# Optimization experiments

Hardware: AMD Instinct MI355X
Metric: run time of the kernel (lower is better)

The kernel has to match this reference:

```python
import jax, jax.numpy as jnp
import numpy as np

EPS = 1e-5
SCALE = 30.0

def _ln(x, g, b):
    m = jnp.mean(x, axis=-1, keepdims=True)
    v = jnp.mean((x - m) ** 2, axis=-1, keepdims=True)
    return (x - m) * jax.lax.rsqrt(v + EPS) * g + b

def setup_inputs() -> dict:
    key = jax.random.key(0)
    ks = jax.random.split(key, 12)
    B, L, K, H, NIN = 4, 2048, 48, 128, 512
    s = 0.02
    return {
        "h_V": jax.random.normal(ks[0], (B, L, H), jnp.float32),
        "h_E": jax.random.normal(ks[1], (B, L, K, NIN - H), jnp.float32),
        "mask_V": jnp.ones((B, L), jnp.float32),
        "mask_E": jnp.ones((B, L, K), jnp.float32),
        "w1": jax.random.normal(ks[2], (NIN, H), jnp.float32) * s,
        "b1": jnp.zeros((H,), jnp.float32),
        "w2": jax.random.normal(ks[3], (H, H), jnp.float32) * s,
        "b2": jnp.zeros((H,), jnp.float32),
        "w3": jax.random.normal(ks[4], (H, H), jnp.float32) * s,
        "b3": jnp.zeros((H,), jnp.float32),
        "g1": jnp.ones((H,), jnp.float32),
        "bn1": jnp.zeros((H,), jnp.float32),
        "g2": jnp.ones((H,), jnp.float32),
        "bn2": jnp.zeros((H,), jnp.float32),
        "wf1": jax.random.normal(ks[5], (H, 4 * H), jnp.float32) * s,
        "bf1": jnp.zeros((4 * H,), jnp.float32),
        "wf2": jax.random.normal(ks[6], (4 * H, H), jnp.float32) * s,
        "bf2": jnp.zeros((H,), jnp.float32),
    }

def reference(h_V, h_E, mask_V, mask_E, w1, b1, w2, b2, w3, b3, g1, bn1, g2, bn2, wf1, bf1, wf2, bf2):
    B, L, H = h_V.shape
    K = h_E.shape[-2]
    gelu = lambda x: jax.nn.gelu(x, approximate=False)  # torch nn.GELU default (erf)
    # expand source node over K neighbors and concat: (B,L,K,num_in)
    h_V_exp = jnp.broadcast_to(h_V[:, :, None, :], (B, L, K, H))
    h_EV = jnp.concatenate([h_V_exp, h_E], axis=-1)
    h_msg = gelu(jnp.einsum('blki,ih->blkh', h_EV, w1) + b1)
    h_msg = gelu(jnp.einsum('blkh,hj->blkj', h_msg, w2) + b2)
    h_msg = jnp.einsum('blkh,hj->blkj', h_msg, w3) + b3
    h_msg = mask_E[..., None] * h_msg
    dh = jnp.sum(h_msg, axis=-2) / SCALE  # masked sum-aggregate over K
    h = _ln(h_V + dh, g1, bn1)
    dff = jnp.einsum('blh,hf->blf', h, wf1) + bf1
    dff = jnp.einsum('blf,fh->blh', gelu(dff), wf2) + bf2
    h = _ln(h + dff, g2, bn2)
    return mask_V[..., None] * h
```

## Files before the change

kernel.cpp:

```cpp
#include <hip/hip_runtime.h>
#include <hip/hip_bf16.h>


typedef __bf16 bf16x8 __attribute__((ext_vector_type(8)));
typedef __bf16 bf16x4 __attribute__((ext_vector_type(4)));
typedef float f32x4 __attribute__((ext_vector_type(4)));

#define HH 128
#define EE 384
#define KK 48

__device__ __forceinline__ float gelu_f(float x) {
  float x2 = x * x;
  float u = x * (-1.5957691216f - 0.0713548163f * x2);
  float e = __expf(u);
  return __fdividef(x, 1.0f + e);
}

__device__ __forceinline__ bf16x8 cvt8v(f32x4 a, f32x4 b) {
  bf16x8 r;
  #pragma unroll
  for (int i = 0; i < 4; ++i) { r[i] = (__bf16)a[i]; r[i + 4] = (__bf16)b[i]; }
  return r;
}

__device__ __forceinline__ f32x4 mfma16(bf16x8 a, bf16x8 b, f32x4 c) {
  return __builtin_amdgcn_mfma_f32_16x16x32_bf16(a, b, c, 0, 0, 0);
}

__device__ __forceinline__ void gload16(const void* g, void* l) {
  __builtin_amdgcn_global_load_lds(
      (const __attribute__((address_space(1))) void*)g,
      (__attribute__((address_space(3))) void*)l, 16, 0, 0);
}

__global__ void prep_kernel(const float* __restrict__ w1, const float* __restrict__ w2,
                            const float* __restrict__ w3, const float* __restrict__ wf1,
                            const float* __restrict__ wf2, __bf16* __restrict__ out) {
  int idx = blockIdx.x * 256 + threadIdx.x;
  if (idx < 49152) {
    int t = idx & 7, lane = (idx >> 3) & 63, n = (idx >> 9) & 7, kc = idx >> 12;
    int e = kc * 32 + (lane >> 4) * 8 + t, h = n * 16 + (lane & 15);
    out[idx] = (__bf16)w1[(128 + e) * 128 + h];
  } else if (idx < 65536) {
    int u = idx - 49152;
    int t = u & 7, lane = (u >> 3) & 63, n = (u >> 9) & 7, kc = u >> 12;
    int e = kc * 32 + (lane >> 4) * 8 + t, h = n * 16 + (lane & 15);
    out[idx] = (__bf16)w2[e * 128 + h];
  } else if (idx < 81920) {
    int u = idx - 65536;
    int t = u & 7, lane = (u >> 3) & 63, n = (u >> 9) & 7, kc = u >> 12;
    int e = kc * 32 + (lane >> 4) * 8 + t, h = n * 16 + (lane & 15);
    out[idx] = (__bf16)w3[e * 128 + h];
  } else if (idx < 147456) {
    int u = idx - 81920;
    int t = u & 7, lane = (u >> 3) & 63, n = (u >> 9) & 7, kc = (u >> 12) & 3, w = u >> 14;
    int f = w * 128 + n * 16 + (lane & 15), h = kc * 32 + (lane >> 4) * 8 + t;
    out[idx] = (__bf16)wf1[h * 512 + f];
  } else if (idx < 212992) {
    int u = idx - 147456;
    int t = u & 7, lane = (u >> 3) & 63, n = (u >> 9) & 1, kc = (u >> 10) & 15, w = u >> 14;
    int j = w * 32 + n * 16 + (lane & 15), f = kc * 32 + (lane >> 4) * 8 + t;
    out[idx] = (__bf16)wf2[f * 128 + j];
  }
}

__global__ __launch_bounds__(128) void v1_kernel(const float* __restrict__ hV,
                                                 const float* __restrict__ w1,
                                                 const float* __restrict__ b1,
                                                 float* __restrict__ V1) {
  __shared__ __align__(16) float sV[16][128];
  const int tid = threadIdx.x;
  const long p0 = (long)blockIdx.x * 16;
  for (int i = 0; i < 16; ++i) sV[i][tid] = hV[(p0 + i) * HH + tid];
  __syncthreads();
  float acc[16];
  float bb = b1[tid];
  #pragma unroll
  for (int p = 0; p < 16; ++p) acc[p] = bb;
  for (int k = 0; k < 128; k += 4) {
    float wa = w1[(k + 0) * HH + tid];
    float wb = w1[(k + 1) * HH + tid];
    float wc = w1[(k + 2) * HH + tid];
    float wd = w1[(k + 3) * HH + tid];
    #pragma unroll
    for (int p = 0; p < 16; ++p) {
      float4 h4 = *(const float4*)&sV[p][k];
      acc[p] = fmaf(h4.x, wa, fmaf(h4.y, wb, fmaf(h4.z, wc, fmaf(h4.w, wd, acc[p]))));
    }
  }
  #pragma unroll
  for (int p = 0; p < 16; ++p) V1[(p0 + p) * HH + tid] = acc[p];
}

__global__ __launch_bounds__(256, 4) void msg_kernel(
    const float* __restrict__ hE, const float* __restrict__ hV,
    const float* __restrict__ maskE,
    const __bf16* __restrict__ w1f, const __bf16* __restrict__ w2f,
    const __bf16* __restrict__ w3f, const float* __restrict__ V1,
    const float* __restrict__ b2, const float* __restrict__ b3,
    const float* __restrict__ g1, const float* __restrict__ bn1,
    float* __restrict__ outH) {
  __shared__ __align__(16) char sBuf[3][12288];
  __shared__ __align__(16) float sBias[512];
  __shared__ __align__(16) float sPart[4][2];

  const int tid = threadIdx.x;
  const int lane = tid & 63;
  const int w = tid >> 6;
  const int fr = lane & 15;
  const int fg = lane >> 4;
  const long p = blockIdx.x;

  for (int j = tid; j < 512; j += 256) {
    float v;
    if (j < 128) v = b2[j];
    else if (j < 256) v = b3[j - 128];
    else if (j < 384) v = g1[j - 256];
    else v = bn1[j - 384];
    sBias[j] = v;
  }
  __syncthreads();

  const float mk0 = maskE[p * KK + fr];
  const float mk1 = maskE[p * KK + 16 + fr];
  const float mk2 = maskE[p * KK + 32 + fr];

  const char* hEp = (const char*)(hE + p * (long)(KK * EE));
  const int lrow = lane >> 4;
  const int lcb = (lane & 15) * 16;
  const int r0 = (w * 3 + 0) * 4 + lrow;
  const int r1 = (w * 3 + 1) * 4 + lrow;
  const int r2 = (w * 3 + 2) * 4 + lrow;
  const char* srcA0 = hEp + r0 * 1536 + (lcb ^ ((r0 & 7) << 5));
  const char* srcA1 = hEp + r1 * 1536 + (lcb ^ ((r1 & 7) << 5));
  const char* srcA2 = hEp + r2 * 1536 + (lcb ^ ((r2 & 7) << 5));
  const int dst0 = (w * 3 + 0) * 1024;
  const int dst1 = (w * 3 + 1) * 1024;
  const int dst2 = (w * 3 + 2) * 1024;

  const __bf16* b1base = w1f + (2 * w) * 512 + lane * 8;
  const __bf16* b2base = w2f + (2 * w) * 512 + lane * 8;
  const __bf16* b3base = w3f + (2 * w) * 512 + lane * 8;

  const int aswz = (fr & 7) << 5;
  const int hswz = (fr & 7) << 4;
  char* hB = &sBuf[0][0];

  f32x4 acc[3][2];
  #pragma unroll
  for (int m = 0; m < 3; ++m)
    #pragma unroll
    for (int n = 0; n < 2; ++n) acc[m][n] = (f32x4){0.f, 0.f, 0.f, 0.f};

  bf16x8 Bs0[2], Bs1[2], Bs2[2], Bs3[2];

#define STAGE(C, BUF) { \
    gload16(srcA0 + (C) * 256, &sBuf[BUF][0] + dst0); \
    gload16(srcA1 + (C) * 256, &sBuf[BUF][0] + dst1); \
    gload16(srcA2 + (C) * 256, &sBuf[BUF][0] + dst2); }
#define LOADB(SET, BASE, KC) { \
    SET[0] = *(const bf16x8*)((BASE) + (KC) * 4096); \
    SET[1] = *(const bf16x8*)((BASE) + (KC) * 4096 + 256); }
#define WAITV(N) asm volatile("s_waitcnt vmcnt(" #N ")" ::: "memory")
#define BAR      asm volatile("s_barrier" ::: "memory")
#define BARL     asm volatile("s_waitcnt lgkmcnt(0)\ns_barrier" ::: "memory")

#define KSTEP(BUF, KS, SET) { \
    const char* rb_ = &sBuf[BUF][0]; \
    const int cb_ = ((KS) * 128 + fg * 32) ^ aswz; \
    f32x4 x0_ = *(const f32x4*)(rb_ + fr * 256 + cb_); \
    f32x4 x1_ = *(const f32x4*)(rb_ + fr * 256 + cb_ + 16); \
    f32x4 x2_ = *(const f32x4*)(rb_ + (16 + fr) * 256 + cb_); \
    f32x4 x3_ = *(const f32x4*)(rb_ + (16 + fr) * 256 + cb_ + 16); \
    f32x4 x4_ = *(const f32x4*)(rb_ + (32 + fr) * 256 + cb_); \
    f32x4 x5_ = *(const f32x4*)(rb_ + (32 + fr) * 256 + cb_ + 16); \
    bf16x8 af0 = cvt8v(x0_, x1_); \
    bf16x8 af1 = cvt8v(x2_, x3_); \
    bf16x8 af2 = cvt8v(x4_, x5_); \
    acc[0][0] = mfma16(SET[0], af0, acc[0][0]); acc[0][1] = mfma16(SET[1], af0, acc[0][1]); \
    acc[1][0] = mfma16(SET[0], af1, acc[1][0]); acc[1][1] = mfma16(SET[1], af1, acc[1][1]); \
    acc[2][0] = mfma16(SET[0], af2, acc[2][0]); acc[2][1] = mfma16(SET[1], af2, acc[2][1]); }

#define KSTEPH(KS, SET) { \
    const int cb_ = ((KS) * 64 + fg * 16) ^ hswz; \
    bf16x8 af0 = *(const bf16x8*)(hB + fr * 256 + cb_); \
    bf16x8 af1 = *(const bf16x8*)(hB + (16 + fr) * 256 + cb_); \
    bf16x8 af2 = *(const bf16x8*)(hB + (32 + fr) * 256 + cb_); \
    acc[0][0] = mfma16(SET[0], af0, acc[0][0]); acc[0][1] = mfma16(SET[1], af0, acc[0][1]); \
    acc[1][0] = mfma16(SET[0], af1, acc[1][0]); acc[1][1] = mfma16(SET[1], af1, acc[1][1]); \
    acc[2][0] = mfma16(SET[0], af2, acc[2][0]); acc[2][1] = mfma16(SET[1], af2, acc[2][1]); }

#define EPI(BQ0, BQ1) { \
    _Pragma("unroll") for (int m_ = 0; m_ < 3; ++m_) { \
      const int rb_ = (m_ * 16 + fr) * 256; \
      { bf16x4 t_; \
        _Pragma("unroll") for (int j_ = 0; j_ < 4; ++j_) t_[j_] = (__bf16)gelu_f(acc[m_][0][j_] + BQ0[j_]); \
        *(bf16x4*)(hB + rb_ + (((2 * w) * 32 + fg * 8) ^ hswz)) = t_; \
        acc[m_][0] = (f32x4){0.f, 0.f, 0.f, 0.f}; } \
      { bf16x4 t_; \
        _Pragma("unroll") for (int j_ = 0; j_ < 4; ++j_) t_[j_] = (__bf16)gelu_f(acc[m_][1][j_] + BQ1[j_]); \
        *(bf16x4*)(hB + rb_ + (((2 * w + 1) * 32 + fg * 8) ^ hswz)) = t_; \
        acc[m_][1] = (f32x4){0.f, 0.f, 0.f, 0.f}; } } }

  STAGE(0, 0);
  LOADB(Bs0, b1base, 0);
  LOADB(Bs1, b1base, 1);
  STAGE(1, 1);
  LOADB(Bs2, b1base, 2);
  LOADB(Bs3, b1base, 3);

  f32x4 vq0, vq1, hq0, hq1;

  WAITV(7); BAR;
  KSTEP(0, 0, Bs0); LOADB(Bs0, b1base, 4);
  KSTEP(0, 1, Bs1); LOADB(Bs1, b1base, 5);
  STAGE(2, 2);

  WAITV(7); BAR;
  KSTEP(1, 0, Bs2); LOADB(Bs2, b1base, 6);
  KSTEP(1, 1, Bs3); LOADB(Bs3, b1base, 7);
  STAGE(3, 0);

  WAITV(7); BAR;
  KSTEP(2, 0, Bs0); LOADB(Bs0, b1base, 8);
  KSTEP(2, 1, Bs1); LOADB(Bs1, b1base, 9);
  STAGE(4, 1);

  WAITV(7); BAR;
  KSTEP(0, 0, Bs2); LOADB(Bs2, b1base, 10);
  KSTEP(0, 1, Bs3); LOADB(Bs3, b1base, 11);
  STAGE(5, 2);

  WAITV(7); BAR;
  KSTEP(1, 0, Bs0); LOADB(Bs0, b2base, 0);
  vq0 = *(const f32x4*)(V1 + p * HH + (2 * w) * 16 + fg * 4);
  vq1 = *(const f32x4*)(V1 + p * HH + (2 * w + 1) * 16 + fg * 4);
  KSTEP(1, 1, Bs1); LOADB(Bs1, b2base, 1);

  WAITV(6); BAR;
  KSTEP(2, 0, Bs2); LOADB(Bs2, b2base, 2);
  KSTEP(2, 1, Bs3); LOADB(Bs3, b2base, 3);

  WAITV(4);
  EPI(vq0, vq1);
  BARL;

  KSTEPH(0, Bs0); LOADB(Bs0, b3base, 0);
  KSTEPH(1, Bs1); LOADB(Bs1, b3base, 1);
  WAITV(4);
  KSTEPH(2, Bs2); LOADB(Bs2, b3base, 2);
  KSTEPH(3, Bs3); LOADB(Bs3, b3base, 3);
  BARL;
  {
    f32x4 bq0 = *(const f32x4*)(&sBias[(2 * w) * 16 + fg * 4]);
    f32x4 bq1 = *(const f32x4*)(&sBias[(2 * w + 1) * 16 + fg * 4]);
    EPI(bq0, bq1);
  }
  BARL;

  WAITV(6);
  KSTEPH(0, Bs0);
  hq0 = *(const f32x4*)(hV + p * HH + (2 * w) * 16 + fg * 4);
  hq1 = *(const f32x4*)(hV + p * HH + (2 * w + 1) * 16 + fg * 4);
  KSTEPH(1, Bs1);
  WAITV(4);
  KSTEPH(2, Bs2);
  KSTEPH(3, Bs3);

  f32x4 red[2];
  {
    #pragma unroll
    for (int n = 0; n < 2; ++n) {
      f32x4 bq = *(const f32x4*)(&sBias[128 + (2 * w + n) * 16 + fg * 4]);
      red[n] = mk0 * (acc[0][n] + bq) + mk1 * (acc[1][n] + bq) + mk2 * (acc[2][n] + bq);
    }
    #pragma unroll
    for (int off = 1; off <= 8; off <<= 1)
      #pragma unroll
      for (int n = 0; n < 2; ++n)
        #pragma unroll
        for (int j = 0; j < 4; ++j)
          red[n][j] += __shfl_xor(red[n][j], off);
  }

  WAITV(0);
  {
    f32x4 xq[2];
    xq[0] = hq0 + red[0] * (1.f / 30.f);
    xq[1] = hq1 + red[1] * (1.f / 30.f);
    float s = 0.f, t = 0.f;
    #pragma unroll
    for (int n = 0; n < 2; ++n)
      #pragma unroll
      for (int j = 0; j < 4; ++j) { float x = xq[n][j]; s += x; t += x * x; }
    s += __shfl_xor(s, 16); s += __shfl_xor(s, 32);
    t += __shfl_xor(t, 16); t += __shfl_xor(t, 32);
    if (lane == 0) { sPart[w][0] = s; sPart[w][1] = t; }
    BARL;
    float S = sPart[0][0] + sPart[1][0] + sPart[2][0] + sPart[3][0];
    float T = sPart[0][1] + sPart[1][1] + sPart[2][1] + sPart[3][1];
    float mean = S * (1.f / 128.f);
    float var = T * (1.f / 128.f) - mean * mean;
    float rs = rsqrtf(var + 1e-5f);
    if (fr == 0) {
      #pragma unroll
      for (int n = 0; n < 2; ++n) {
        f32x4 gq = *(const f32x4*)(&sBias[256 + (2 * w + n) * 16 + fg * 4]);
        f32x4 bq = *(const f32x4*)(&sBias[384 + (2 * w + n) * 16 + fg * 4]);
        f32x4 o;
        #pragma unroll
        for (int j = 0; j < 4; ++j) o[j] = (xq[n][j] - mean) * rs * gq[j] + bq[j];
        *(f32x4*)(outH + p * HH + (2 * w + n) * 16 + fg * 4) = o;
      }
    }
  }
#undef STAGE
#undef LOADB
#undef WAITV
#undef BAR
#undef BARL
#undef KSTEP
#undef KSTEPH
#undef EPI
}

__global__ __launch_bounds__(256, 2) void ffn_kernel(
    const float* __restrict__ xin, const __bf16* __restrict__ wf1g,
    const float* __restrict__ bf1, const __bf16* __restrict__ wf2g,
    const float* __restrict__ bf2, const float* __restrict__ g2,
    const float* __restrict__ bn2, const float* __restrict__ maskV,
    float* __restrict__ out) {
  __shared__ __align__(16) __bf16 sX[16][136];
  __shared__ __align__(16) __bf16 sH1[16][520];
  __shared__ __align__(16) float sOut[16][132];
  const int tid = threadIdx.x, lane = tid & 63, w = tid >> 6;
  const long row0 = (long)blockIdx.x * 16;
  const int fr = lane & 15, fg = lane >> 4;
  const __bf16* bw1 = wf1g + w * 16384 + lane * 8;
  const __bf16* bw2 = wf2g + w * 16384 + lane * 8;

  {
    int r = tid >> 4, c = (tid & 15) * 8;
    const float* src = xin + (row0 + r) * HH + c;
    f32x4 v0 = *(const f32x4*)src, v1 = *(const f32x4*)(src + 4);
    *(bf16x8*)&sX[r][c] = cvt8v(v0, v1);
  }
  __syncthreads();

  f32x4 a1[8];
  #pragma unroll
  for (int n = 0; n < 8; ++n) a1[n] = (f32x4){0.f, 0.f, 0.f, 0.f};
  #pragma unroll
  for (int kc = 0; kc < 4; ++kc) {
    int k0 = kc * 32;
    bf16x8 af0 = *(const bf16x8*)&sX[fr][k0 + fg * 8];
    #pragma unroll
    for (int n = 0; n < 8; ++n) {
      bf16x8 bfr = *(const bf16x8*)(bw1 + (kc * 8 + n) * 512);
      a1[n] = mfma16(af0, bfr, a1[n]);
    }
  }
  #pragma unroll
  for (int n = 0; n < 8; ++n) {
    float bv = bf1[w * 128 + n * 16 + fr];
    #pragma unroll
    for (int j = 0; j < 4; ++j)
      sH1[fg * 4 + j][w * 128 + n * 16 + fr] = (__bf16)gelu_f(a1[n][j] + bv);
  }
  __syncthreads();

  f32x4 a2[2];
  #pragma unroll
  for (int n = 0; n < 2; ++n) a2[n] = (f32x4){0.f, 0.f, 0.f, 0.f};
  #pragma unroll
  for (int kc = 0; kc < 16; ++kc) {
    int k0 = kc * 32;
    bf16x8 af0 = *(const bf16x8*)&sH1[fr][k0 + fg * 8];
    #pragma unroll
    for (int n = 0; n < 2; ++n) {
      bf16x8 bfr = *(const bf16x8*)(bw2 + (kc * 2 + n) * 512);
      a2[n] = mfma16(af0, bfr, a2[n]);
    }
  }
  #pragma unroll
  for (int n = 0; n < 2; ++n) {
    float bv = bf2[w * 32 + n * 16 + fr];
    #pragma unroll
    for (int j = 0; j < 4; ++j)
      sOut[fg * 4 + j][w * 32 + n * 16 + fr] = a2[n][j] + bv;
  }
  __syncthreads();

  {
    int r = tid >> 4, c0 = (tid & 15) * 8;
    long p = row0 + r;
    const float* xp = xin + p * HH + c0;
    float x[8];
    #pragma unroll
    for (int i = 0; i < 8; ++i) x[i] = xp[i] + sOut[r][c0 + i];
    float s = 0.f;
    #pragma unroll
    for (int i = 0; i < 8; ++i) s += x[i];
    s += __shfl_xor(s, 1); s += __shfl_xor(s, 2); s += __shfl_xor(s, 4); s += __shfl_xor(s, 8);
    float mean = s * (1.f / 128.f);
    float q = 0.f;
    #pragma unroll
    for (int i = 0; i < 8; ++i) { float e = x[i] - mean; q += e * e; }
    q += __shfl_xor(q, 1); q += __shfl_xor(q, 2); q += __shfl_xor(q, 4); q += __shfl_xor(q, 8);
    float rs = rsqrtf(q * (1.f / 128.f) + 1e-5f);
    float mv = maskV[p];
    float* op = out + p * HH + c0;
    #pragma unroll
    for (int i = 0; i < 8; ++i)
      op[i] = ((x[i] - mean) * rs * g2[c0 + i] + bn2[c0 + i]) * mv;
  }
}

extern "C" void kernel_launch(void* const* d_in, const int* in_sizes, int n_in,
                              void* d_out, int out_size, void* d_ws, size_t ws_size,
                              hipStream_t stream) {
  const float* hV    = (const float*)d_in[0];
  const float* hE    = (const float*)d_in[1];
  const float* maskV = (const float*)d_in[2];
  const float* maskE = (const float*)d_in[3];
  const float* w1    = (const float*)d_in[4];
  const float* b1    = (const float*)d_in[5];
  const float* w2    = (const float*)d_in[6];
  const float* b2    = (const float*)d_in[7];
  const float* w3    = (const float*)d_in[8];
  const float* b3    = (const float*)d_in[9];
  const float* g1    = (const float*)d_in[10];
  const float* bn1   = (const float*)d_in[11];
  const float* g2    = (const float*)d_in[12];
  const float* bn2   = (const float*)d_in[13];
  const float* wf1   = (const float*)d_in[14];
  const float* bf1   = (const float*)d_in[15];
  const float* wf2   = (const float*)d_in[16];
  const float* bf2   = (const float*)d_in[17];
  float* out = (float*)d_out;

  __bf16* wsb = (__bf16*)d_ws;
  float* V1   = (float*)((char*)d_ws + 425984);
  float* hbuf = (float*)((char*)d_ws + 4620288);

  prep_kernel<<<832, 256, 0, stream>>>(w1, w2, w3, wf1, wf2, wsb);
  v1_kernel<<<512, 128, 0, stream>>>(hV, w1, b1, V1);
  msg_kernel<<<8192, 256, 0, stream>>>(hE, hV, maskE,
                                       wsb, wsb + 49152, wsb + 65536, V1,
                                       b2, b3, g1, bn1, hbuf);
  ffn_kernel<<<512, 256, 0, stream>>>(hbuf, wsb + 81920, bf1, wsb + 147456, bf2,
                                      g2, bn2, maskV, out);
}
```

Before: 200.2 us.

## Split message kernel into layer-1 and layers-2/3 kernels via bf16 workspace

Splits the fused message MLP kernel into two kernels. The first streams h_E, computes layer 1 plus GELU and writes the bf16 hidden activations to a workspace buffer. The second processes four positions per block, keeping the W2 and W3 fragments in registers and double-buffering the hidden tiles. The point is to stop reloading W2/W3 for every position and to let each phase run at its own occupancy. The cost is an extra global round-trip of about 100MB of bf16 intermediates. The split path is used only when the workspace is large enough, otherwise the original fused kernel runs.

```diff
diff --git a/kernel.cpp b/kernel.cpp
--- a/kernel.cpp
+++ b/kernel.cpp
@@ -93,69 +93,7 @@
   for (int p = 0; p < 16; ++p) V1[(p0 + p) * HH + tid] = acc[p];
 }
 
-__global__ __launch_bounds__(256, 4) void msg_kernel(
-    const float* __restrict__ hE, const float* __restrict__ hV,
-    const float* __restrict__ maskE,
-    const __bf16* __restrict__ w1f, const __bf16* __restrict__ w2f,
-    const __bf16* __restrict__ w3f, const float* __restrict__ V1,
-    const float* __restrict__ b2, const float* __restrict__ b3,
-    const float* __restrict__ g1, const float* __restrict__ bn1,
-    float* __restrict__ outH) {
-  __shared__ __align__(16) char sBuf[3][12288];
-  __shared__ __align__(16) float sBias[512];
-  __shared__ __align__(16) float sPart[4][2];
-
-  const int tid = threadIdx.x;
-  const int lane = tid & 63;
-  const int w = tid >> 6;
-  const int fr = lane & 15;
-  const int fg = lane >> 4;
-  const long p = blockIdx.x;
-
-  for (int j = tid; j < 512; j += 256) {
-    float v;
-    if (j < 128) v = b2[j];
-    else if (j < 256) v = b3[j - 128];
-    else if (j < 384) v = g1[j - 256];
-    else v = bn1[j - 384];
-    sBias[j] = v;
-  }
-  __syncthreads();
-
-  const float mk0 = maskE[p * KK + fr];
-  const float mk1 = maskE[p * KK + 16 + fr];
-  const float mk2 = maskE[p * KK + 32 + fr];
-
-  const char* hEp = (const char*)(hE + p * (long)(KK * EE));
-  const int lrow = lane >> 4;
-  const int lcb = (lane & 15) * 16;
-  const int r0 = (w * 3 + 0) * 4 + lrow;
-  const int r1 = (w * 3 + 1) * 4 + lrow;
-  const int r2 = (w * 3 + 2) * 4 + lrow;
-  const char* srcA0 = hEp + r0 * 1536 + (lcb ^ ((r0 & 7) << 5));
-  const char* srcA1 = hEp + r1 * 1536 + (lcb ^ ((r1 & 7) << 5));
-  const char* srcA2 = hEp + r2 * 1536 + (lcb ^ ((r2 & 7) << 5));
-  const int dst0 = (w * 3 + 0) * 1024;
-  const int dst1 = (w * 3 + 1) * 1024;
-  const int dst2 = (w * 3 + 2) * 1024;
-
-  const __bf16* b1base = w1f + (2 * w) * 512 + lane * 8;
-  const __bf16* b2base = w2f + (2 * w) * 512 + lane * 8;
-  const __bf16* b3base = w3f + (2 * w) * 512 + lane * 8;
-
-  const int aswz = (fr & 7) << 5;
-  const int hswz = (fr & 7) << 4;
-  char* hB = &sBuf[0][0];
-
-  f32x4 acc[3][2];
-  #pragma unroll
-  for (int m = 0; m < 3; ++m)
-    #pragma unroll
-    for (int n = 0; n < 2; ++n) acc[m][n] = (f32x4){0.f, 0.f, 0.f, 0.f};
-
-  bf16x8 Bs0[2], Bs1[2], Bs2[2], Bs3[2];
-
-#define STAGE(C, BUF) { \
+#define STAGEM(C, BUF) { \
     gload16(srcA0 + (C) * 256, &sBuf[BUF][0] + dst0); \
     gload16(srcA1 + (C) * 256, &sBuf[BUF][0] + dst1); \
     gload16(srcA2 + (C) * 256, &sBuf[BUF][0] + dst2); }
@@ -165,8 +103,7 @@
 #define WAITV(N) asm volatile("s_waitcnt vmcnt(" #N ")" ::: "memory")
 #define BAR      asm volatile("s_barrier" ::: "memory")
 #define BARL     asm volatile("s_waitcnt lgkmcnt(0)\ns_barrier" ::: "memory")
-
-#define KSTEP(BUF, KS, SET) { \
+#define KSTEPM(BUF, KS, SET) { \
     const char* rb_ = &sBuf[BUF][0]; \
     const int cb_ = ((KS) * 128 + fg * 32) ^ aswz; \
     f32x4 x0_ = *(const f32x4*)(rb_ + fr * 256 + cb_); \
@@ -181,92 +118,341 @@
     acc[0][0] = mfma16(SET[0], af0, acc[0][0]); acc[0][1] = mfma16(SET[1], af0, acc[0][1]); \
     acc[1][0] = mfma16(SET[0], af1, acc[1][0]); acc[1][1] = mfma16(SET[1], af1, acc[1][1]); \
     acc[2][0] = mfma16(SET[0], af2, acc[2][0]); acc[2][1] = mfma16(SET[1], af2, acc[2][1]); }
-
-#define KSTEPH(KS, SET) { \
+#define KSTEPH2(HB, KS, SET) { \
     const int cb_ = ((KS) * 64 + fg * 16) ^ hswz; \
-    bf16x8 af0 = *(const bf16x8*)(hB + fr * 256 + cb_); \
-    bf16x8 af1 = *(const bf16x8*)(hB + (16 + fr) * 256 + cb_); \
-    bf16x8 af2 = *(const bf16x8*)(hB + (32 + fr) * 256 + cb_); \
+    bf16x8 af0 = *(const bf16x8*)((HB) + fr * 256 + cb_); \
+    bf16x8 af1 = *(const bf16x8*)((HB) + (16 + fr) * 256 + cb_); \
+    bf16x8 af2 = *(const bf16x8*)((HB) + (32 + fr) * 256 + cb_); \
     acc[0][0] = mfma16(SET[0], af0, acc[0][0]); acc[0][1] = mfma16(SET[1], af0, acc[0][1]); \
     acc[1][0] = mfma16(SET[0], af1, acc[1][0]); acc[1][1] = mfma16(SET[1], af1, acc[1][1]); \
     acc[2][0] = mfma16(SET[0], af2, acc[2][0]); acc[2][1] = mfma16(SET[1], af2, acc[2][1]); }
-
-#define EPI(BQ0, BQ1) { \
+#define EPI2(HB, BQ0, BQ1) { \
     _Pragma("unroll") for (int m_ = 0; m_ < 3; ++m_) { \
       const int rb_ = (m_ * 16 + fr) * 256; \
       { bf16x4 t_; \
         _Pragma("unroll") for (int j_ = 0; j_ < 4; ++j_) t_[j_] = (__bf16)gelu_f(acc[m_][0][j_] + BQ0[j_]); \
-        *(bf16x4*)(hB + rb_ + (((2 * w) * 32 + fg * 8) ^ hswz)) = t_; \
+        *(bf16x4*)((HB) + rb_ + (((2 * w) * 32 + fg * 8) ^ hswz)) = t_; \
         acc[m_][0] = (f32x4){0.f, 0.f, 0.f, 0.f}; } \
       { bf16x4 t_; \
         _Pragma("unroll") for (int j_ = 0; j_ < 4; ++j_) t_[j_] = (__bf16)gelu_f(acc[m_][1][j_] + BQ1[j_]); \
-        *(bf16x4*)(hB + rb_ + (((2 * w + 1) * 32 + fg * 8) ^ hswz)) = t_; \
+        *(bf16x4*)((HB) + rb_ + (((2 * w + 1) * 32 + fg * 8) ^ hswz)) = t_; \
         acc[m_][1] = (f32x4){0.f, 0.f, 0.f, 0.f}; } } }
 
-  STAGE(0, 0);
+__global__ __launch_bounds__(256, 4) void msg1_kernel(
+    const float* __restrict__ hE, const __bf16* __restrict__ w1f,
+    const float* __restrict__ V1, char* __restrict__ h1g) {
+  __shared__ __align__(16) char sBuf[3][12288];
+  const int tid = threadIdx.x;
+  const int lane = tid & 63;
+  const int w = tid >> 6;
+  const int fr = lane & 15;
+  const int fg = lane >> 4;
+  const long p = blockIdx.x;
+
+  const char* hEp = (const char*)(hE + p * (long)(KK * EE));
+  const int lrow = lane >> 4;
+  const int lcb = (lane & 15) * 16;
+  const int r0 = (w * 3 + 0) * 4 + lrow;
+  const int r1 = (w * 3 + 1) * 4 + lrow;
+  const int r2 = (w * 3 + 2) * 4 + lrow;
+  const char* srcA0 = hEp + r0 * 1536 + (lcb ^ ((r0 & 7) << 5));
+  const char* srcA1 = hEp + r1 * 1536 + (lcb ^ ((r1 & 7) << 5));
+  const char* srcA2 = hEp + r2 * 1536 + (lcb ^ ((r2 & 7) << 5));
+  const int dst0 = (w * 3 + 0) * 1024;
+  const int dst1 = (w * 3 + 1) * 1024;
+  const int dst2 = (w * 3 + 2) * 1024;
+  const __bf16* b1base = w1f + (2 * w) * 512 + lane * 8;
+  const int aswz = (fr & 7) << 5;
+  const int hswz = (fr & 7) << 4;
+  char* hB = &sBuf[0][0];
+
+  f32x4 acc[3][2];
+  #pragma unroll
+  for (int m = 0; m < 3; ++m)
+    #pragma unroll
+    for (int n = 0; n < 2; ++n) acc[m][n] = (f32x4){0.f, 0.f, 0.f, 0.f};
+  bf16x8 Bs0[2], Bs1[2], Bs2[2], Bs3[2];
+
+  STAGEM(0, 0);
   LOADB(Bs0, b1base, 0);
   LOADB(Bs1, b1base, 1);
-  STAGE(1, 1);
+  STAGEM(1, 1);
   LOADB(Bs2, b1base, 2);
   LOADB(Bs3, b1base, 3);
 
-  f32x4 vq0, vq1, hq0, hq1;
-
-  WAITV(7); BAR;
-  KSTEP(0, 0, Bs0); LOADB(Bs0, b1base, 4);
-  KSTEP(0, 1, Bs1); LOADB(Bs1, b1base, 5);
-  STAGE(2, 2);
-
-  WAITV(7); BAR;
-  KSTEP(1, 0, Bs2); LOADB(Bs2, b1base, 6);
-  KSTEP(1, 1, Bs3); LOADB(Bs3, b1base, 7);
-  STAGE(3, 0);
-
-  WAITV(7); BAR;
-  KSTEP(2, 0, Bs0); LOADB(Bs0, b1base, 8);
-  KSTEP(2, 1, Bs1); LOADB(Bs1, b1base, 9);
-  STAGE(4, 1);
-
-  WAITV(7); BAR;
-  KSTEP(0, 0, Bs2); LOADB(Bs2, b1base, 10);
-  KSTEP(0, 1, Bs3); LOADB(Bs3, b1base, 11);
-  STAGE(5, 2);
-
-  WAITV(7); BAR;
-  KSTEP(1, 0, Bs0); LOADB(Bs0, b2base, 0);
+  f32x4 vq0, vq1;
+
+  WAITV(7); BAR;
+  KSTEPM(0, 0, Bs0); LOADB(Bs0, b1base, 4);
+  KSTEPM(0, 1, Bs1); LOADB(Bs1, b1base, 5);
+  STAGEM(2, 2);
+  WAITV(7); BAR;
+  KSTEPM(1, 0, Bs2); LOADB(Bs2, b1base, 6);
+  KSTEPM(1, 1, Bs3); LOADB(Bs3, b1base, 7);
+  STAGEM(3, 0);
+  WAITV(7); BAR;
+  KSTEPM(2, 0, Bs0); LOADB(Bs0, b1base, 8);
+  KSTEPM(2, 1, Bs1); LOADB(Bs1, b1base, 9);
+  STAGEM(4, 1);
+  WAITV(7); BAR;
+  KSTEPM(0, 0, Bs2); LOADB(Bs2, b1base, 10);
+  KSTEPM(0, 1, Bs3); LOADB(Bs3, b1base, 11);
+  STAGEM(5, 2);
+  WAITV(7); BAR;
+  KSTEPM(1, 0, Bs0);
   vq0 = *(const f32x4*)(V1 + p * HH + (2 * w) * 16 + fg * 4);
   vq1 = *(const f32x4*)(V1 + p * HH + (2 * w + 1) * 16 + fg * 4);
-  KSTEP(1, 1, Bs1); LOADB(Bs1, b2base, 1);
-
+  KSTEPM(1, 1, Bs1);
+  WAITV(2); BAR;
+  KSTEPM(2, 0, Bs2);
+  KSTEPM(2, 1, Bs3);
+
+  WAITV(0);
+  EPI2(hB, vq0, vq1);
+  BARL;
+
+  {
+    char* dst = h1g + p * 12288;
+    #pragma unroll
+    for (int q = 0; q < 3; ++q) {
+      const int off = w * 3072 + q * 1024 + lane * 16;
+      f32x4 v = *(const f32x4*)(hB + off);
+      *(f32x4*)(dst + off) = v;
+    }
+  }
+}
+
+__global__ __launch_bounds__(256, 3) void msg2_kernel(
+    const char* __restrict__ h1g, const float* __restrict__ hV,
+    const float* __restrict__ maskE,
+    const __bf16* __restrict__ w2f, const __bf16* __restrict__ w3f,
+    const float* __restrict__ b2, const float* __restrict__ b3,
+    const float* __restrict__ g1, const float* __restrict__ bn1,
+    float* __restrict__ outH) {
+  __shared__ __align__(16) char sB[2][12288];
+  __shared__ __align__(16) float sBias[512];
+  __shared__ __align__(16) float sPart[4][2];
+  const int tid = threadIdx.x;
+  const int lane = tid & 63;
+  const int w = tid >> 6;
+  const int fr = lane & 15;
+  const int fg = lane >> 4;
+  const long pbase = (long)blockIdx.x * 4;
+
+  for (int j = tid; j < 512; j += 256) {
+    float v;
+    if (j < 128) v = b2[j];
+    else if (j < 256) v = b3[j - 128];
+    else if (j < 384) v = g1[j - 256];
+    else v = bn1[j - 384];
+    sBias[j] = v;
+  }
+  __syncthreads();
+
+  const __bf16* b2base = w2f + (2 * w) * 512 + lane * 8;
+  const __bf16* b3base = w3f + (2 * w) * 512 + lane * 8;
+  const int hswz = (fr & 7) << 4;
+
+  bf16x8 W20[2], W21[2], W22[2], W23[2], W30[2], W31[2], W32[2], W33[2];
+  LOADB(W20, b2base, 0); LOADB(W21, b2base, 1); LOADB(W22, b2base, 2); LOADB(W23, b2base, 3);
+  LOADB(W30, b3base, 0); LOADB(W31, b3base, 1); LOADB(W32, b3base, 2); LOADB(W33, b3base, 3);
+
+  f32x4 acc[3][2];
+  #pragma unroll
+  for (int m = 0; m < 3; ++m)
+    #pragma unroll
+    for (int n = 0; n < 2; ++n) acc[m][n] = (f32x4){0.f, 0.f, 0.f, 0.f};
+
+#define STAGE2(PP, BUF) { \
+    _Pragma("unroll") for (int q_ = 0; q_ < 3; ++q_) \
+      gload16(h1g + (PP) * 12288 + w * 3072 + q_ * 1024 + lane * 16, \
+              &sB[BUF][0] + w * 3072 + q_ * 1024); }
+
+  STAGE2(pbase, 0);
+
+#define POSBODY(I, CUR, DOSTAGE, REDW) { \
+    const long p = pbase + I; \
+    WAITV(0); BAR; \
+    f32x4 hq0 = *(const f32x4*)(hV + p * HH + (2 * w) * 16 + fg * 4); \
+    f32x4 hq1 = *(const f32x4*)(hV + p * HH + (2 * w + 1) * 16 + fg * 4); \
+    const float mk0 = maskE[p * KK + fr]; \
+    const float mk1 = maskE[p * KK + 16 + fr]; \
+    const float mk2 = maskE[p * KK + 32 + fr]; \
+    if (DOSTAGE) STAGE2(p + 1, (CUR) ^ 1); \
+    char* hB = &sB[CUR][0]; \
+    KSTEPH2(hB, 0, W20); KSTEPH2(hB, 1, W21); KSTEPH2(hB, 2, W22); KSTEPH2(hB, 3, W23); \
+    BARL; \
+    { f32x4 bq0 = *(const f32x4*)(&sBias[(2 * w) * 16 + fg * 4]); \
+      f32x4 bq1 = *(const f32x4*)(&sBias[(2 * w + 1) * 16 + fg * 4]); \
+      EPI2(hB, bq0, bq1); } \
+    BARL; \
+    KSTEPH2(hB, 0, W30); KSTEPH2(hB, 1, W31); KSTEPH2(hB, 2, W32); KSTEPH2(hB, 3, W33); \
+    WAITV(REDW); \
+    f32x4 red[2]; \
+    _Pragma("unroll") for (int n_ = 0; n_ < 2; ++n_) { \
+      f32x4 bq_ = *(const f32x4*)(&sBias[128 + (2 * w + n_) * 16 + fg * 4]); \
+      red[n_] = mk0 * (acc[0][n_] + bq_) + mk1 * (acc[1][n_] + bq_) + mk2 * (acc[2][n_] + bq_); \
+      acc[0][n_] = (f32x4){0.f, 0.f, 0.f, 0.f}; \
+      acc[1][n_] = (f32x4){0.f, 0.f, 0.f, 0.f}; \
+      acc[2][n_] = (f32x4){0.f, 0.f, 0.f, 0.f}; } \
+    _Pragma("unroll") for (int off_ = 1; off_ <= 8; off_ <<= 1) \
+      _Pragma("unroll") for (int n_ = 0; n_ < 2; ++n_) \
+        _Pragma("unroll") for (int j_ = 0; j_ < 4; ++j_) \
+          red[n_][j_] += __shfl_xor(red[n_][j_], off_); \
+    f32x4 xq[2]; \
+    xq[0] = hq0 + red[0] * (1.f / 30.f); \
+    xq[1] = hq1 + red[1] * (1.f / 30.f); \
+    float s_ = 0.f, t_ = 0.f; \
+    _Pragma("unroll") for (int n_ = 0; n_ < 2; ++n_) \
+      _Pragma("unroll") for (int j_ = 0; j_ < 4; ++j_) { float x_ = xq[n_][j_]; s_ += x_; t_ += x_ * x_; } \
+    s_ += __shfl_xor(s_, 16); s_ += __shfl_xor(s_, 32); \
+    t_ += __shfl_xor(t_, 16); t_ += __shfl_xor(t_, 32); \
+    if (lane == 0) { sPart[w][0] = s_; sPart[w][1] = t_; } \
+    BARL; \
+    float S_ = sPart[0][0] + sPart[1][0] + sPart[2][0] + sPart[3][0]; \
+    float T_ = sPart[0][1] + sPart[1][1] + sPart[2][1] + sPart[3][1]; \
+    float mean_ = S_ * (1.f / 128.f); \
+    float var_ = T_ * (1.f / 128.f) - mean_ * mean_; \
+    float rs_ = rsqrtf(var_ + 1e-5f); \
+    if (fr == 0) { \
+      _Pragma("unroll") for (int n_ = 0; n_ < 2; ++n_) { \
+        f32x4 gq_ = *(const f32x4*)(&sBias[256 + (2 * w + n_) * 16 + fg * 4]); \
+        f32x4 bq_ = *(const f32x4*)(&sBias[384 + (2 * w + n_) * 16 + fg * 4]); \
+        f32x4 o_; \
+        _Pragma("unroll") for (int j_ = 0; j_ < 4; ++j_) \
+          o_[j_] = (xq[n_][j_] - mean_) * rs_ * gq_[j_] + bq_[j_]; \
+        *(f32x4*)(outH + p * HH + (2 * w + n_) * 16 + fg * 4) = o_; } } }
+
+  POSBODY(0, 0, 1, 3);
+  POSBODY(1, 1, 1, 3);
+  POSBODY(2, 0, 1, 3);
+  POSBODY(3, 1, 0, 0);
+
+#undef STAGE2
+#undef POSBODY
+}
+
+__global__ __launch_bounds__(256, 4) void msg_kernel(
+    const float* __restrict__ hE, const float* __restrict__ hV,
+    const float* __restrict__ maskE,
+    const __bf16* __restrict__ w1f, const __bf16* __restrict__ w2f,
+    const __bf16* __restrict__ w3f, const float* __restrict__ V1,
+    const float* __restrict__ b2, const float* __restrict__ b3,
+    const float* __restrict__ g1, const float* __restrict__ bn1,
+    float* __restrict__ outH) {
+  __shared__ __align__(16) char sBuf[3][12288];
+  __shared__ __align__(16) float sBias[512];
+  __shared__ __align__(16) float sPart[4][2];
+
+  const int tid = threadIdx.x;
+  const int lane = tid & 63;
+  const int w = tid >> 6;
+  const int fr = lane & 15;
+  const int fg = lane >> 4;
+  const long p = blockIdx.x;
+
+  for (int j = tid; j < 512; j += 256) {
+    float v;
+    if (j < 128) v = b2[j];
+    else if (j < 256) v = b3[j - 128];
+    else if (j < 384) v = g1[j - 256];
+    else v = bn1[j - 384];
+    sBias[j] = v;
+  }
+  __syncthreads();
+
+  const float mk0 = maskE[p * KK + fr];
+  const float mk1 = maskE[p * KK + 16 + fr];
+  const float mk2 = maskE[p * KK + 32 + fr];
+
+  const char* hEp = (const char*)(hE + p * (long)(KK * EE));
+  const int lrow = lane >> 4;
+  const int lcb = (lane & 15) * 16;
+  const int r0 = (w * 3 + 0) * 4 + lrow;
+  const int r1 = (w * 3 + 1) * 4 + lrow;
+  const int r2 = (w * 3 + 2) * 4 + lrow;
+  const char* srcA0 = hEp + r0 * 1536 + (lcb ^ ((r0 & 7) << 5));
+  const char* srcA1 = hEp + r1 * 1536 + (lcb ^ ((r1 & 7) << 5));
+  const char* srcA2 = hEp + r2 * 1536 + (lcb ^ ((r2 & 7) << 5));
+  const int dst0 = (w * 3 + 0) * 1024;
+  const int dst1 = (w * 3 + 1) * 1024;
+  const int dst2 = (w * 3 + 2) * 1024;
+
+  const __bf16* b1base = w1f + (2 * w) * 512 + lane * 8;
+  const __bf16* b2base = w2f + (2 * w) * 512 + lane * 8;
+  const __bf16* b3base = w3f + (2 * w) * 512 + lane * 8;
+
+  const int aswz = (fr & 7) << 5;
+  const int hswz = (fr & 7) << 4;
+  char* hB = &sBuf[0][0];
+
+  f32x4 acc[3][2];
+  #pragma unroll
+  for (int m = 0; m < 3; ++m)
+    #pragma unroll
+    for (int n = 0; n < 2; ++n) acc[m][n] = (f32x4){0.f, 0.f, 0.f, 0.f};
+
+  bf16x8 Bs0[2], Bs1[2], Bs2[2], Bs3[2];
+
+  STAGEM(0, 0);
+  LOADB(Bs0, b1base, 0);
+  LOADB(Bs1, b1base, 1);
+  STAGEM(1, 1);
+  LOADB(Bs2, b1base, 2);
+  LOADB(Bs3, b1base, 3);
+
+  f32x4 vq0, vq1, hq0, hq1;
+
+  WAITV(7); BAR;
+  KSTEPM(0, 0, Bs0); LOADB(Bs0, b1base, 4);
+  KSTEPM(0, 1, Bs1); LOADB(Bs1, b1base, 5);
+  STAGEM(2, 2);
+  WAITV(7); BAR;
+  KSTEPM(1, 0, Bs2); LOADB(Bs2, b1base, 6);
+  KSTEPM(1, 1, Bs3); LOADB(Bs3, b1base, 7);
+  STAGEM(3, 0);
+  WAITV(7); BAR;
+  KSTEPM(2, 0, Bs0); LOADB(Bs0, b1base, 8);
+  KSTEPM(2, 1, Bs1); LOADB(Bs1, b1base, 9);
+  STAGEM(4, 1);
+  WAITV(7); BAR;
+  KSTEPM(0, 0, Bs2); LOADB(Bs2, b1base, 10);
+  KSTEPM(0, 1, Bs3); LOADB(Bs3, b1base, 11);
+  STAGEM(5, 2);
+  WAITV(7); BAR;
+  KSTEPM(1, 0, Bs0); LOADB(Bs0, b2base, 0);
+  vq0 = *(const f32x4*)(V1 + p * HH + (2 * w) * 16 + fg * 4);
+  vq1 = *(const f32x4*)(V1 + p * HH + (2 * w + 1) * 16 + fg * 4);
+  KSTEPM(1, 1, Bs1); LOADB(Bs1, b2base, 1);
   WAITV(6); BAR;
-  KSTEP(2, 0, Bs2); LOADB(Bs2, b2base, 2);
-  KSTEP(2, 1, Bs3); LOADB(Bs3, b2base, 3);
+  KSTEPM(2, 0, Bs2); LOADB(Bs2, b2base, 2);
+  KSTEPM(2, 1, Bs3); LOADB(Bs3, b2base, 3);
 
   WAITV(4);
-  EPI(vq0, vq1);
+  EPI2(hB, vq0, vq1);
   BARL;
 
-  KSTEPH(0, Bs0); LOADB(Bs0, b3base, 0);
-  KSTEPH(1, Bs1); LOADB(Bs1, b3base, 1);
+  KSTEPH2(hB, 0, Bs0); LOADB(Bs0, b3base, 0);
+  KSTEPH2(hB, 1, Bs1); LOADB(Bs1, b3base, 1);
   WAITV(4);
-  KSTEPH(2, Bs2); LOADB(Bs2, b3base, 2);
-  KSTEPH(3, Bs3); LOADB(Bs3, b3base, 3);
+  KSTEPH2(hB, 2, Bs2); LOADB(Bs2, b3base, 2);
+  KSTEPH2(hB, 3, Bs3); LOADB(Bs3, b3base, 3);
   BARL;
   {
     f32x4 bq0 = *(const f32x4*)(&sBias[(2 * w) * 16 + fg * 4]);
     f32x4 bq1 = *(const f32x4*)(&sBias[(2 * w + 1) * 16 + fg * 4]);
-    EPI(bq0, bq1);
+    EPI2(hB, bq0, bq1);
   }
   BARL;
 
   WAITV(6);
-  KSTEPH(0, Bs0);
+  KSTEPH2(hB, 0, Bs0);
   hq0 = *(const f32x4*)(hV + p * HH + (2 * w) * 16 + fg * 4);
   hq1 = *(const f32x4*)(hV + p * HH + (2 * w + 1) * 16 + fg * 4);
-  KSTEPH(1, Bs1);
+  KSTEPH2(hB, 1, Bs1);
   WAITV(4);
-  KSTEPH(2, Bs2);
-  KSTEPH(3, Bs3);
+  KSTEPH2(hB, 2, Bs2);
+  KSTEPH2(hB, 3, Bs3);
 
   f32x4 red[2];
   {
@@ -315,14 +501,6 @@
       }
     }
   }
-#undef STAGE
-#undef LOADB
-#undef WAITV
-#undef BAR
-#undef BARL
-#undef KSTEP
-#undef KSTEPH
-#undef EPI
 }
 
 __global__ __launch_bounds__(256, 2) void ffn_kernel(
@@ -443,12 +621,21 @@
   __bf16* wsb = (__bf16*)d_ws;
   float* V1   = (float*)((char*)d_ws + 425984);
   float* hbuf = (float*)((char*)d_ws + 4620288);
+  char*  h1g  = (char*)d_ws + 8814592;
 
   prep_kernel<<<832, 256, 0, stream>>>(w1, w2, w3, wf1, wf2, wsb);
   v1_kernel<<<512, 128, 0, stream>>>(hV, w1, b1, V1);
-  msg_kernel<<<8192, 256, 0, stream>>>(hE, hV, maskE,
-                                       wsb, wsb + 49152, wsb + 65536, V1,
-                                       b2, b3, g1, bn1, hbuf);
+
+  const bool split = ws_size >= 109477888ull;
+  if (split) {
+    msg1_kernel<<<8192, 256, 0, stream>>>(hE, wsb, V1, h1g);
+    msg2_kernel<<<2048, 256, 0, stream>>>(h1g, hV, maskE, wsb + 49152, wsb + 65536,
+                                          b2, b3, g1, bn1, hbuf);
+  } else {
+    msg_kernel<<<8192, 256, 0, stream>>>(hE, hV, maskE,
+                                         wsb, wsb + 49152, wsb + 65536, V1,
+                                         b2, b3, g1, bn1, hbuf);
+  }
   ffn_kernel<<<512, 256, 0, stream>>>(hbuf, wsb + 81920, bf1, wsb + 147456, bf2,
                                       g2, bn2, maskV, out);
 }
```

Measured after the change: 241.3 us. 1.21x slower.
